# Kernel optimization log

Hardware: AMD Instinct MI355X
Metric: run time of the kernel (lower is better)

The kernel has to match this reference:

```python
import jax, jax.numpy as jnp
import numpy as np

N_NODES = 100000


def setup_inputs() -> dict:
    key = jax.random.key(0)
    k1, k2, k3, k4, k5, k6 = jax.random.split(key, 6)
    n_edges = 1_000_000
    d_in, d_out = 64, 64
    x = jax.random.normal(k1, (N_NODES, d_in), dtype=jnp.float32)
    edge_row = jax.random.randint(k2, (n_edges,), 0, N_NODES, dtype=jnp.int64)
    edge_col = jax.random.randint(k3, (n_edges,), 0, N_NODES, dtype=jnp.int64)
    edge_val = jax.random.uniform(k4, (n_edges,), dtype=jnp.float32)
    W = jax.random.normal(k5, (d_out, d_in), dtype=jnp.float32) / jnp.sqrt(d_in)
    b = jax.random.normal(k6, (d_out,), dtype=jnp.float32)
    return {"x": x, "edge_row": edge_row, "edge_col": edge_col,
            "edge_val": edge_val, "W": W, "b": b}


def reference(x, edge_row, edge_col, edge_val, W, b):
    # SpMM: agg[i] = sum_{e: row[e]==i} val[e] * x[col[e]]
    msgs = edge_val[:, None] * x[edge_col]              # [E, d_in]
    agg = jax.ops.segment_sum(msgs, edge_row, num_segments=N_NODES)  # [N, d_in]
    # nn.Linear: agg @ W.T + b
    return agg @ W.T + b
```

## Files before the change

### kernel.cpp

```cpp
#include <hip/hip_runtime.h>

#define N_NODES 100000
#define D 64
#define BIN_ROWS 64
#define NBINS 1563
#define PE 2048
#define NTILES 6250
#define XB 391

typedef unsigned int u32;
typedef __attribute__((ext_vector_type(8))) short short8;
typedef __attribute__((ext_vector_type(4))) float f32x4;

__device__ __forceinline__ float bf16_to_f32(unsigned short u) {
    union { u32 i; float f; } c; c.i = ((u32)u) << 16; return c.f;
}
__device__ __forceinline__ unsigned short f32_to_bf16(float f) {
    union { float f; u32 i; } c; c.f = f;
    const u32 u = c.i;
    return (unsigned short)((u + 0x7FFFu + ((u >> 16) & 1u)) >> 16);
}
__device__ __forceinline__ short8 pack_bf16x8(float4 a, float4 b) {
    short8 r;
    r[0] = (short)f32_to_bf16(a.x); r[1] = (short)f32_to_bf16(a.y);
    r[2] = (short)f32_to_bf16(a.z); r[3] = (short)f32_to_bf16(a.w);
    r[4] = (short)f32_to_bf16(b.x); r[5] = (short)f32_to_bf16(b.y);
    r[6] = (short)f32_to_bf16(b.z); r[7] = (short)f32_to_bf16(b.w);
    return r;
}

__global__ __launch_bounds__(512) void hist_kernel(const int* __restrict__ erow,
                                                   int* __restrict__ hist2d, int ne) {
    __shared__ int h[NBINS];
    const int tid = threadIdx.x;
    for (int i = tid; i < NBINS; i += 512) h[i] = 0;
    __syncthreads();
    const int base = blockIdx.x * PE;
    const int end  = min(base + PE, ne);
    for (int e = base + tid; e < end; e += 512)
        atomicAdd(&h[erow[e] >> 6], 1);
    __syncthreads();
    for (int i = tid; i < NBINS; i += 512)
        hist2d[blockIdx.x * NBINS + i] = h[i];
}

__global__ __launch_bounds__(256) void scanA_kernel(const int* __restrict__ hist2d,
                                                    int* __restrict__ scan2d,
                                                    int* __restrict__ bsum,
                                                    int total, int npb) {
    __shared__ int sdat[256];
    const int tid  = threadIdx.x;
    const int base = blockIdx.x * 1024 + tid * 4;
    int v[4], sum = 0;
    int bin = 0, blk = 0;
    if (base < total) { bin = base / npb; blk = base - bin * npb; }
#pragma unroll
    for (int k = 0; k < 4; ++k) {
        const int idx = base + k;
        v[k] = (idx < total) ? hist2d[blk * NBINS + bin] : 0;
        sum += v[k];
        if (++blk == npb) { blk = 0; ++bin; }
    }
    sdat[tid] = sum;
    __syncthreads();
    for (int d = 1; d < 256; d <<= 1) {
        const int t = (tid >= d) ? sdat[tid - d] : 0;
        __syncthreads();
        sdat[tid] += t;
        __syncthreads();
    }
    int run = sdat[tid] - sum;
#pragma unroll
    for (int k = 0; k < 4; ++k) {
        const int idx = base + k;
        if (idx < total) scan2d[idx] = run;
        run += v[k];
    }
    if (tid == 255) bsum[blockIdx.x] = sdat[255];
}

__global__ __launch_bounds__(1024) void scanB_kernel(int* __restrict__ bsum, int nb) {
    __shared__ int s[1024];
    const int tid = threadIdx.x;
    const int a = (2 * tid     < nb) ? bsum[2 * tid]     : 0;
    const int b = (2 * tid + 1 < nb) ? bsum[2 * tid + 1] : 0;
    const int pair = a + b;
    s[tid] = pair;
    __syncthreads();
    for (int d = 1; d < 1024; d <<= 1) {
        const int t = (tid >= d) ? s[tid - d] : 0;
        __syncthreads();
        s[tid] += t;
        __syncthreads();
    }
    const int excl = s[tid] - pair;
    if (2 * tid     < nb) bsum[2 * tid]     = excl;
    if (2 * tid + 1 < nb) bsum[2 * tid + 1] = excl + a;
}

__global__ __launch_bounds__(256) void xw_part_kernel(const float* __restrict__ x,
                                                      const float* __restrict__ W,
                                                      unsigned short* __restrict__ y,
                                                      const int* __restrict__ erow,
                                                      const int* __restrict__ ecol,
                                                      const float* __restrict__ eval_,
                                                      const int* __restrict__ scan2d,
                                                      const int* __restrict__ bsum,
                                                      u32* __restrict__ pedge,
                                                      int* __restrict__ binStart,
                                                      int ne, int npb) {
    __shared__ int lcur[NBINS];
    const int tid = threadIdx.x;

    if ((int)blockIdx.x < npb) {
        const int blk = blockIdx.x;
        for (int i = tid; i < NBINS; i += 256) {
            const int idx = i * npb + blk;
            const int v = scan2d[idx] + bsum[idx >> 10];
            lcur[i] = v;
            if (blk == 0) binStart[i] = v;
        }
        if (blk == 0 && tid == 0) binStart[NBINS] = ne;
        __syncthreads();
        const int base = blk * PE;
        const int end  = min(base + PE, ne);
        for (int e = base + tid; e < end; e += 256) {
            const int r   = erow[e];
            const int bin = r >> 6;
            const int pos = atomicAdd(&lcur[bin], 1);
            int q = (int)(eval_[e] * 512.0f + 0.5f);
            q = (q > 511) ? 511 : q;
            pedge[pos] = ((u32)ecol[e] << 15) | ((u32)(r & 63) << 9) | (u32)q;
        }
        return;
    }

    const int gw = ((int)blockIdx.x - npb) * 4 + (tid >> 6);
    const int c  = tid & 15;
    const int q4 = (tid >> 4) & 3;

    const float4* Wv = (const float4*)W;
    short8 bfrag[4][2];
#pragma unroll
    for (int g = 0; g < 4; ++g) {
#pragma unroll
        for (int h = 0; h < 2; ++h) {
            const int bi = (16 * g + c) * 16 + 8 * h + 2 * q4;
            bfrag[g][h] = pack_bf16x8(((const float4*)Wv)[bi], ((const float4*)Wv)[bi + 1]);
        }
    }

    const float4* Xv = (const float4*)x;
#pragma unroll
    for (int t = 0; t < 4; ++t) {
        const int tile = gw + 1564 * t;
        if (tile >= NTILES) break;
        const int n0 = tile * 16;

        const int ai = (n0 + c) * 16 + 2 * q4;
        const short8 a0 = pack_bf16x8(Xv[ai],     Xv[ai + 1]);
        const short8 a1 = pack_bf16x8(Xv[ai + 8], Xv[ai + 9]);

        f32x4 acc0 = {0.f, 0.f, 0.f, 0.f}, acc1 = acc0, acc2 = acc0, acc3 = acc0;
        acc0 = __builtin_amdgcn_mfma_f32_16x16x32_bf16(a0, bfrag[0][0], acc0, 0, 0, 0);
        acc1 = __builtin_amdgcn_mfma_f32_16x16x32_bf16(a0, bfrag[1][0], acc1, 0, 0, 0);
        acc2 = __builtin_amdgcn_mfma_f32_16x16x32_bf16(a0, bfrag[2][0], acc2, 0, 0, 0);
        acc3 = __builtin_amdgcn_mfma_f32_16x16x32_bf16(a0, bfrag[3][0], acc3, 0, 0, 0);
        acc0 = __builtin_amdgcn_mfma_f32_16x16x32_bf16(a1, bfrag[0][1], acc0, 0, 0, 0);
        acc1 = __builtin_amdgcn_mfma_f32_16x16x32_bf16(a1, bfrag[1][1], acc1, 0, 0, 0);
        acc2 = __builtin_amdgcn_mfma_f32_16x16x32_bf16(a1, bfrag[2][1], acc2, 0, 0, 0);
        acc3 = __builtin_amdgcn_mfma_f32_16x16x32_bf16(a1, bfrag[3][1], acc3, 0, 0, 0);

        const int rbase = n0 + q4 * 4;
#pragma unroll
        for (int r = 0; r < 4; ++r) {
            y[(rbase + r) * D +  0 + c] = f32_to_bf16(acc0[r]);
            y[(rbase + r) * D + 16 + c] = f32_to_bf16(acc1[r]);
            y[(rbase + r) * D + 32 + c] = f32_to_bf16(acc2[r]);
            y[(rbase + r) * D + 48 + c] = f32_to_bf16(acc3[r]);
        }
    }
}

__global__ __launch_bounds__(512) void aggregate_kernel(const int* __restrict__ binStart,
                                                        const u32* __restrict__ pedge,
                                                        const unsigned short* __restrict__ y,
                                                        const float* __restrict__ b,
                                                        float4* __restrict__ out4) {
    __shared__ int acc[BIN_ROWS * D];
    const int tid = threadIdx.x;
    for (int i = tid; i < BIN_ROWS * D; i += 512) acc[i] = 0;
    __syncthreads();

    const int bin  = blockIdx.x;
    const int lane = tid & 63;
    const int w    = tid >> 6;
    const int s    = binStart[bin];
    const int e    = binStart[bin + 1];

    for (int bb0 = s + w * 16; bb0 < e; bb0 += 128) {
        const int bb = __builtin_amdgcn_readfirstlane(bb0);
        u32 u[16];
        if (bb + 16 <= e) {
#pragma unroll
            for (int j = 0; j < 16; ++j) u[j] = pedge[bb + j];
        } else {
#pragma unroll
            for (int j = 0; j < 16; ++j) {
                const int idx = bb + j;
                u[j] = (idx < e) ? pedge[idx] : 0u;
            }
        }
        unsigned short g[16];
#pragma unroll
        for (int j = 0; j < 16; ++j) {
            g[j] = y[(int)(u[j] >> 15) * D + lane];
        }
#pragma unroll
        for (int j = 0; j < 16; ++j) {
            const float vq = (float)(u[j] & 511u);
            const float yf = bf16_to_f32(g[j]);
            const int   qi = (int)(vq * yf * 512.0f);
            const int   r  = (int)((u[j] >> 9) & 63u);
            atomicAdd(&acc[r * D + lane], qi);
        }
    }
    __syncthreads();

    const int rowBase = bin * BIN_ROWS;
    const float INV = 1.0f / 262144.0f;
    for (int i = tid; i < BIN_ROWS * 16; i += 512) {
        const int rl = i >> 4, q = i & 15;
        const int row = rowBase + rl;
        if (row < N_NODES) {
            const int4   a  = ((const int4*)acc)[i];
            const float4 bv = ((const float4*)b)[q];
            out4[row * 16 + q] = make_float4((float)a.x * INV + bv.x,
                                             (float)a.y * INV + bv.y,
                                             (float)a.z * INV + bv.z,
                                             (float)a.w * INV + bv.w);
        }
    }
}

__global__ __launch_bounds__(256) void init_out_kernel(const float* __restrict__ b,
                                                       float* __restrict__ out) {
    const int i = blockIdx.x * blockDim.x + threadIdx.x;
    const int total4 = N_NODES * D / 4;
    if (i < total4) {
        const float4* b4 = reinterpret_cast<const float4*>(b);
        reinterpret_cast<float4*>(out)[i] = b4[i & 15];
    }
}

__global__ __launch_bounds__(256) void scatter_kernel(const int* __restrict__ erow,
                                                      const int* __restrict__ ecol,
                                                      const float* __restrict__ eval_,
                                                      const unsigned short* __restrict__ y,
                                                      float* __restrict__ out, int ne) {
    const int e    = blockIdx.x * 4 + (threadIdx.x >> 6);
    const int lane = threadIdx.x & 63;
    if (e >= ne) return;
    atomicAdd(&out[erow[e] * D + lane], eval_[e] * bf16_to_f32(y[ecol[e] * D + lane]));
}

extern "C" void kernel_launch(void* const* d_in, const int* in_sizes, int n_in,
                              void* d_out, int out_size, void* d_ws, size_t ws_size,
                              hipStream_t stream) {
    const float* x     = (const float*)d_in[0];
    const int*   erow  = (const int*)  d_in[1];
    const int*   ecol  = (const int*)  d_in[2];
    const float* eval_ = (const float*)d_in[3];
    const float* W     = (const float*)d_in[4];
    const float* b     = (const float*)d_in[5];
    float*       out   = (float*)d_out;
    const int ne = in_sizes[1];

    char* ws = (char*)d_ws;
    const size_t Y_OFF     = 0;
    const size_t PEDGE_OFF = 12800000;
    const size_t H2D_OFF   = 16800000;
    const size_t SCAN_OFF  = 20800000;
    const size_t BSUM_OFF  = 24800000;
    const size_t BST_OFF   = 24808192;
    const size_t TOTAL     = 24814592;

    unsigned short* y = (unsigned short*)(ws + Y_OFF);

    const int npb      = (ne + PE - 1) / PE;
    const int totalSc  = NBINS * npb;
    const int nblocksA = (totalSc + 1023) / 1024;

    if (ws_size >= TOTAL && npb <= 1341) {
        u32* pedge    = (u32*)(ws + PEDGE_OFF);
        int* hist2d   = (int*)(ws + H2D_OFF);
        int* scan2d   = (int*)(ws + SCAN_OFF);
        int* bsum     = (int*)(ws + BSUM_OFF);
        int* binStart = (int*)(ws + BST_OFF);

        hist_kernel<<<npb, 512, 0, stream>>>(erow, hist2d, ne);

        scanA_kernel<<<nblocksA, 256, 0, stream>>>(hist2d, scan2d, bsum, totalSc, npb);
        scanB_kernel<<<1, 1024, 0, stream>>>(bsum, nblocksA);

        xw_part_kernel<<<npb + XB, 256, 0, stream>>>(x, W, y, erow, ecol, eval_,
                                                     scan2d, bsum, pedge, binStart, ne, npb);

        aggregate_kernel<<<NBINS, 512, 0, stream>>>(binStart, pedge, y, b, (float4*)out);
    } else {
        xw_part_kernel<<<XB, 256, 0, stream>>>(x, W, y, erow, ecol, eval_,
                                               (int*)ws, (int*)ws, (u32*)ws, (int*)ws, 0, 0);
        init_out_kernel<<<(N_NODES * D / 4 + 255) / 256, 256, 0, stream>>>(b, out);
        scatter_kernel<<<(ne + 3) / 4, 256, 0, stream>>>(erow, ecol, eval_, y, out, ne);
    }
}
```

Baseline: 67.01 us.

## Replace single-level 1563-bin counting sort with two-level coarse-then-fine bucketing

The edge partition now counts edges into 196 coarse buckets of 512 rows instead of 1563 fine bins of 64 rows. This shrinks the per-block histogram and the 2D scan, roughly by a factor of eight. A new pass2 kernel then splits each coarse bucket into its 8 fine bins with an LDS counting sort. That adds an extra read and write of 8-byte packed edges and one more kernel launch, in exchange for a much smaller scan and histogram workload.

```diff
diff --git a/kernel.cpp b/kernel.cpp
--- a/kernel.cpp
+++ b/kernel.cpp
@@ -4,6 +4,7 @@
 #define D 64
 #define BIN_ROWS 64
 #define NBINS 1563
+#define NC 196
 #define PE 2048
 #define NTILES 6250
 #define XB 391
@@ -29,37 +30,36 @@
     return r;
 }
 
-__global__ __launch_bounds__(512) void hist_kernel(const int* __restrict__ erow,
-                                                   int* __restrict__ hist2d, int ne) {
-    __shared__ int h[NBINS];
-    const int tid = threadIdx.x;
-    for (int i = tid; i < NBINS; i += 512) h[i] = 0;
+__global__ __launch_bounds__(512) void histC_kernel(const int* __restrict__ erow,
+                                                    int* __restrict__ coarse2d, int ne) {
+    __shared__ int h[NC];
+    const int tid = threadIdx.x;
+    if (tid < NC) h[tid] = 0;
     __syncthreads();
     const int base = blockIdx.x * PE;
     const int end  = min(base + PE, ne);
     for (int e = base + tid; e < end; e += 512)
-        atomicAdd(&h[erow[e] >> 6], 1);
-    __syncthreads();
-    for (int i = tid; i < NBINS; i += 512)
-        hist2d[blockIdx.x * NBINS + i] = h[i];
-}
-
-__global__ __launch_bounds__(256) void scanA_kernel(const int* __restrict__ hist2d,
-                                                    int* __restrict__ scan2d,
+        atomicAdd(&h[erow[e] >> 9], 1);
+    __syncthreads();
+    if (tid < NC) coarse2d[blockIdx.x * NC + tid] = h[tid];
+}
+
+__global__ __launch_bounds__(256) void scanA_kernel(const int* __restrict__ coarse2d,
+                                                    int* __restrict__ csc,
                                                     int* __restrict__ bsum,
                                                     int total, int npb) {
     __shared__ int sdat[256];
     const int tid  = threadIdx.x;
     const int base = blockIdx.x * 1024 + tid * 4;
     int v[4], sum = 0;
-    int bin = 0, blk = 0;
-    if (base < total) { bin = base / npb; blk = base - bin * npb; }
+    int C = 0, blk = 0;
+    if (base < total) { C = base / npb; blk = base - C * npb; }
 #pragma unroll
     for (int k = 0; k < 4; ++k) {
         const int idx = base + k;
-        v[k] = (idx < total) ? hist2d[blk * NBINS + bin] : 0;
+        v[k] = (idx < total) ? coarse2d[blk * NC + C] : 0;
         sum += v[k];
-        if (++blk == npb) { blk = 0; ++bin; }
+        if (++blk == npb) { blk = 0; ++C; }
     }
     sdat[tid] = sum;
     __syncthreads();
@@ -73,7 +73,7 @@
 #pragma unroll
     for (int k = 0; k < 4; ++k) {
         const int idx = base + k;
-        if (idx < total) scan2d[idx] = run;
+        if (idx < total) csc[idx] = run;
         run += v[k];
     }
     if (tid == 255) bsum[blockIdx.x] = sdat[255];
@@ -98,39 +98,42 @@
     if (2 * tid + 1 < nb) bsum[2 * tid + 1] = excl + a;
 }
 
-__global__ __launch_bounds__(256) void xw_part_kernel(const float* __restrict__ x,
-                                                      const float* __restrict__ W,
-                                                      unsigned short* __restrict__ y,
-                                                      const int* __restrict__ erow,
-                                                      const int* __restrict__ ecol,
-                                                      const float* __restrict__ eval_,
-                                                      const int* __restrict__ scan2d,
-                                                      const int* __restrict__ bsum,
-                                                      u32* __restrict__ pedge,
-                                                      int* __restrict__ binStart,
-                                                      int ne, int npb) {
-    __shared__ int lcur[NBINS];
+__global__ __launch_bounds__(256) void xw_pass1_kernel(const float* __restrict__ x,
+                                                       const float* __restrict__ W,
+                                                       unsigned short* __restrict__ y,
+                                                       const int* __restrict__ erow,
+                                                       const int* __restrict__ ecol,
+                                                       const float* __restrict__ eval_,
+                                                       const int* __restrict__ csc,
+                                                       const int* __restrict__ bsum,
+                                                       uint2* __restrict__ pedge1,
+                                                       int* __restrict__ cstart,
+                                                       int ne, int npb) {
+    __shared__ int lcur[NC];
     const int tid = threadIdx.x;
 
     if ((int)blockIdx.x < npb) {
         const int blk = blockIdx.x;
-        for (int i = tid; i < NBINS; i += 256) {
-            const int idx = i * npb + blk;
-            const int v = scan2d[idx] + bsum[idx >> 10];
-            lcur[i] = v;
-            if (blk == 0) binStart[i] = v;
-        }
-        if (blk == 0 && tid == 0) binStart[NBINS] = ne;
+        if (tid < NC) {
+            const int idx = tid * npb + blk;
+            const int v = csc[idx] + bsum[idx >> 10];
+            lcur[tid] = v;
+            if (blk == 0) cstart[tid] = v;
+        }
+        if (blk == 0 && tid == 0) cstart[NC] = ne;
         __syncthreads();
         const int base = blk * PE;
         const int end  = min(base + PE, ne);
         for (int e = base + tid; e < end; e += 256) {
-            const int r   = erow[e];
-            const int bin = r >> 6;
-            const int pos = atomicAdd(&lcur[bin], 1);
+            const int r = erow[e];
+            const int C = r >> 9;
+            const int pos = atomicAdd(&lcur[C], 1);
             int q = (int)(eval_[e] * 512.0f + 0.5f);
             q = (q > 511) ? 511 : q;
-            pedge[pos] = ((u32)ecol[e] << 15) | ((u32)(r & 63) << 9) | (u32)q;
+            uint2 pk;
+            pk.x = ((u32)ecol[e] << 15) | ((u32)(r & 63) << 9) | (u32)q;
+            pk.y = (u32)((r >> 6) & 7);
+            pedge1[pos] = pk;
         }
         return;
     }
@@ -146,7 +149,7 @@
 #pragma unroll
         for (int h = 0; h < 2; ++h) {
             const int bi = (16 * g + c) * 16 + 8 * h + 2 * q4;
-            bfrag[g][h] = pack_bf16x8(((const float4*)Wv)[bi], ((const float4*)Wv)[bi + 1]);
+            bfrag[g][h] = pack_bf16x8(Wv[bi], Wv[bi + 1]);
         }
     }
 
@@ -179,6 +182,40 @@
             y[(rbase + r) * D + 32 + c] = f32_to_bf16(acc2[r]);
             y[(rbase + r) * D + 48 + c] = f32_to_bf16(acc3[r]);
         }
+    }
+}
+
+__global__ __launch_bounds__(512) void pass2_kernel(const uint2* __restrict__ pedge1,
+                                                    const int* __restrict__ cstart,
+                                                    u32* __restrict__ pedge,
+                                                    int* __restrict__ binStart) {
+    __shared__ int fh[8];
+    __shared__ int fcur[8];
+    const int tid = threadIdx.x;
+    const int C   = blockIdx.x;
+    const int s   = cstart[C];
+    const int e   = cstart[C + 1];
+
+    if (tid < 8) fh[tid] = 0;
+    __syncthreads();
+    for (int i = s + tid; i < e; i += 512)
+        atomicAdd(&fh[pedge1[i].y], 1);
+    __syncthreads();
+    if (tid == 0) {
+        int run = s;
+#pragma unroll
+        for (int j = 0; j < 8; ++j) {
+            fcur[j] = run;
+            binStart[8 * C + j] = run;
+            run += fh[j];
+        }
+        binStart[8 * C + 8] = run;
+    }
+    __syncthreads();
+    for (int i = s + tid; i < e; i += 512) {
+        const uint2 p = pedge1[i];
+        const int pos = atomicAdd(&fcur[p.y], 1);
+        pedge[pos] = p.x;
     }
 }
 
@@ -277,39 +314,45 @@
     const int ne = in_sizes[1];
 
     char* ws = (char*)d_ws;
-    const size_t Y_OFF     = 0;
-    const size_t PEDGE_OFF = 12800000;
-    const size_t H2D_OFF   = 16800000;
-    const size_t SCAN_OFF  = 20800000;
-    const size_t BSUM_OFF  = 24800000;
-    const size_t BST_OFF   = 24808192;
-    const size_t TOTAL     = 24814592;
+    const size_t Y_OFF      = 0;
+    const size_t PEDGE_OFF  = 12800000;
+    const size_t PEDGE1_OFF = 16800000;
+    const size_t C2D_OFF    = 24800000;
+    const size_t CSC_OFF    = 25200000;
+    const size_t BSUM_OFF   = 25600000;
+    const size_t CST_OFF    = 25600512;
+    const size_t BST_OFF    = 25601536;
+    const size_t TOTAL      = 25607936;
 
     unsigned short* y = (unsigned short*)(ws + Y_OFF);
 
     const int npb      = (ne + PE - 1) / PE;
-    const int totalSc  = NBINS * npb;
+    const int totalSc  = NC * npb;
     const int nblocksA = (totalSc + 1023) / 1024;
 
-    if (ws_size >= TOTAL && npb <= 1341) {
-        u32* pedge    = (u32*)(ws + PEDGE_OFF);
-        int* hist2d   = (int*)(ws + H2D_OFF);
-        int* scan2d   = (int*)(ws + SCAN_OFF);
-        int* bsum     = (int*)(ws + BSUM_OFF);
-        int* binStart = (int*)(ws + BST_OFF);
-
-        hist_kernel<<<npb, 512, 0, stream>>>(erow, hist2d, ne);
-
-        scanA_kernel<<<nblocksA, 256, 0, stream>>>(hist2d, scan2d, bsum, totalSc, npb);
+    if (ws_size >= TOTAL && npb <= 510 && ne <= 1000000) {
+        u32*   pedge    = (u32*)  (ws + PEDGE_OFF);
+        uint2* pedge1   = (uint2*)(ws + PEDGE1_OFF);
+        int*   coarse2d = (int*)  (ws + C2D_OFF);
+        int*   csc      = (int*)  (ws + CSC_OFF);
+        int*   bsum     = (int*)  (ws + BSUM_OFF);
+        int*   cstart   = (int*)  (ws + CST_OFF);
+        int*   binStart = (int*)  (ws + BST_OFF);
+
+        histC_kernel<<<npb, 512, 0, stream>>>(erow, coarse2d, ne);
+
+        scanA_kernel<<<nblocksA, 256, 0, stream>>>(coarse2d, csc, bsum, totalSc, npb);
         scanB_kernel<<<1, 1024, 0, stream>>>(bsum, nblocksA);
 
-        xw_part_kernel<<<npb + XB, 256, 0, stream>>>(x, W, y, erow, ecol, eval_,
-                                                     scan2d, bsum, pedge, binStart, ne, npb);
+        xw_pass1_kernel<<<npb + XB, 256, 0, stream>>>(x, W, y, erow, ecol, eval_,
+                                                      csc, bsum, pedge1, cstart, ne, npb);
+
+        pass2_kernel<<<NC, 512, 0, stream>>>(pedge1, cstart, pedge, binStart);
 
         aggregate_kernel<<<NBINS, 512, 0, stream>>>(binStart, pedge, y, b, (float4*)out);
     } else {
-        xw_part_kernel<<<XB, 256, 0, stream>>>(x, W, y, erow, ecol, eval_,
-                                               (int*)ws, (int*)ws, (u32*)ws, (int*)ws, 0, 0);
+        xw_pass1_kernel<<<XB, 256, 0, stream>>>(x, W, y, erow, ecol, eval_,
+                                                (int*)ws, (int*)ws, (uint2*)ws, (int*)ws, 0, 0);
         init_out_kernel<<<(N_NODES * D / 4 + 255) / 256, 256, 0, stream>>>(b, out);
         scatter_kernel<<<(ne + 3) / 4, 256, 0, stream>>>(erow, ecol, eval_, y, out, ne);
     }
```

Result: faster. 65.19 us (-2.7%).
